# Kernel optimization log

Hardware: AMD Instinct MI355X
Metric: run time of the kernel (lower is better)

## Reference

```python
import jax, jax.numpy as jnp
import numpy as np

NUM_HEADS = 8
ROPE_MIN_LOG = -12.0
ROPE_MAX_LOG = 0.0
EPS = 1e-6


def rms_norm(h, w):
    # per-head-dim RMSNorm in fp32 (Qwen3 style), no shift applied in forward
    dt = h.dtype
    h32 = h.astype(jnp.float32)
    var = jnp.mean(h32 * h32, axis=-1, keepdims=True)
    return (w * (h32 * jax.lax.rsqrt(var + EPS))).astype(dt)


def setup_inputs() -> dict:
    key = jax.random.key(0)
    k1, k2, k3 = jax.random.split(key, 3)
    B, H, W, C = 1, 256, 256, 512
    x = jax.random.normal(k1, (B, H, W, C), dtype=jnp.float32)
    w_qkv = jax.random.normal(k2, (3 * C, C), dtype=jnp.float32) * 0.02
    hd = C // NUM_HEADS
    q_norm_w = jnp.ones((hd,), dtype=jnp.float32)
    k_norm_w = jnp.ones((hd,), dtype=jnp.float32)
    w_proj = jax.random.normal(k3, (C, C), dtype=jnp.float32) * 0.02
    b_proj = jnp.zeros((C,), dtype=jnp.float32)
    return {"x": x, "w_qkv": w_qkv, "q_norm_w": q_norm_w, "k_norm_w": k_norm_w,
            "w_proj": w_proj, "b_proj": b_proj}


def reference(x, w_qkv, q_norm_w, k_norm_w, w_proj, b_proj):
    B, H, W, C = x.shape
    nh = NUM_HEADS
    hd = C // nh
    rope_dim = (hd // 2) * 2
    half = rope_dim // 2
    scale = hd ** -0.5

    # [B,H,W,C] -> [B*W, H, C]
    xr = jnp.transpose(x, (0, 2, 1, 3)).reshape(B * W, H, C)
    qkv = jnp.einsum('bhc,dc->bhd', xr, w_qkv)                # [BW, H, 3C]
    qkv = qkv.reshape(B * W, H, 3, nh, hd)
    qkv = jnp.transpose(qkv, (2, 0, 3, 1, 4))                 # [3, BW, nh, H, hd]
    q, k, v = qkv[0], qkv[1], qkv[2]

    q = rms_norm(q, q_norm_w)
    k = rms_norm(k, k_norm_w)

    # segmented-exponential RoPE along trace axis H (default normalized pos)
    pos = jnp.linspace(0.0, 1.0, H, dtype=jnp.float32)        # [H]
    freqs = jnp.exp(jnp.linspace(ROPE_MIN_LOG, ROPE_MAX_LOG, half, dtype=jnp.float32))
    ang = pos[:, None] * freqs[None, :] * jnp.float32(H)      # [H, half]
    cos = jnp.cos(ang)
    sin = jnp.sin(ang)

    def rope(t):
        rot = t[..., :rope_dim].reshape(B * W, nh, H, half, 2)
        te, to = rot[..., 0], rot[..., 1]
        e2 = te * cos - to * sin
        o2 = te * sin + to * cos
        rot2 = jnp.stack([e2, o2], axis=-1).reshape(B * W, nh, H, rope_dim)
        return jnp.concatenate([rot2, t[..., rope_dim:]], axis=-1)

    q = rope(q)
    k = rope(k)

    # SDPA (non-causal, no dropout)
    scores = jnp.einsum('bnqd,bnkd->bnqk', q, k) * scale      # [BW, nh, H, H]
    attn = jax.nn.softmax(scores, axis=-1)
    o = jnp.einsum('bnqk,bnkd->bnqd', attn, v)                # [BW, nh, H, hd]

    o = jnp.transpose(o, (0, 2, 1, 3)).reshape(B * W, H, C)
    out = jnp.einsum('bhc,dc->bhd', o, w_proj) + b_proj
    out = out.reshape(B, W, H, C)
    return jnp.transpose(out, (0, 2, 1, 3))                   # [B, H, W, C]
```

## Files before the change

kernel.cpp:

```cpp
#include <hip/hip_runtime.h>
#include <hip/hip_bf16.h>
#include <cstdint>
#include <cstddef>

#define SEQ 256
#define WDIM 256
#define CDIM 512
#define NHEAD 8
#define HD 64
#define NTOK (SEQ*WDIM)
#define NTT 8

typedef __attribute__((ext_vector_type(8))) short bf16x8;
typedef __attribute__((ext_vector_type(4))) float f32x4;

static __device__ __forceinline__ unsigned short f2bf(float f) {
  __hip_bfloat16 h = __float2bfloat16(f);
  return *reinterpret_cast<unsigned short*>(&h);
}

__global__ void k_convert(const float* __restrict__ x,
                          const float* __restrict__ wqkv,
                          const float* __restrict__ wproj,
                          unsigned short* __restrict__ xb,
                          unsigned short* __restrict__ wqb,
                          unsigned short* __restrict__ wpb) {
  const int NX = NTOK*CDIM/4, NQ = 3*CDIM*CDIM/4, NP = CDIM*CDIM/4;
  const int total = NX + NQ + NP;
  for (int i = blockIdx.x*blockDim.x + threadIdx.x; i < total; i += gridDim.x*blockDim.x) {
    const float4* s; unsigned short* d; int j;
    if (i < NX)           { s = (const float4*)x;     d = xb;  j = i; }
    else if (i < NX+NQ)   { s = (const float4*)wqkv;  d = wqb; j = i-NX; }
    else                  { s = (const float4*)wproj; d = wpb; j = i-NX-NQ; }
    float4 f = s[j];
    ushort4 o;
    o.x = f2bf(f.x); o.y = f2bf(f.y); o.z = f2bf(f.z); o.w = f2bf(f.w);
    ((ushort4*)d)[j] = o;
  }
}

__global__ void k_rope(float2* __restrict__ tab) {
  int i = blockIdx.x*blockDim.x + threadIdx.x;
  if (i >= SEQ*32) return;
  int h = i >> 5, j = i & 31;
  float freq = expf(-12.0f + 12.0f*(float)j/31.0f);
  float ang = ((float)h/255.0f) * freq * 256.0f;
  tab[i] = make_float2(cosf(ang), sinf(ang));
}


#define STAGE_G(tau_, part_)                                                              \
  if ((tau_) < NTT) {                                                                     \
    const int buf_ = (tau_) & 1;                                                          \
    const int ab_ = (part_) >> 1, hh_ = (part_) & 1;                                      \
    const unsigned short* src_ = ab_ ? B : A;                                             \
    const int row0_ = (ab_ ? rowB0 : rowA0) + hh_*128;                                    \
    _Pragma("unroll")                                                                     \
    for (int c_ = 0; c_ < 2; ++c_) {                                                      \
      int G_ = wid*128 + c_*64 + lane;                                                    \
      int r_ = G_ >> 3, g_ = G_ & 7;                                                      \
      int gsw_ = g_ ^ (r_ & 7);                                                           \
      __builtin_amdgcn_global_load_lds(                                                   \
        (const __attribute__((address_space(1))) unsigned int*)                           \
          ((const char*)src_ + (size_t)(row0_ + r_)*1024 + (size_t)(tau_)*128 + gsw_*16), \
        (__attribute__((address_space(3))) unsigned int*)                                 \
          ((char*)&L[buf_][ab_][hh_][0] + G_*16),                                         \
        16, 0, 0);                                                                        \
    }                                                                                     \
  }

#define LDA_(dst, m_, kk_)                                                                 \
  { int r_ = (m_)*16 + li;                                                                 \
    dst = *(const bf16x8*)((const char*)&L[buf][0][wr][0] + r_*128 + (((((kk_)*4)+lg) ^ (r_ & 7))<<4)); }
#define LDB_(dst, n_, kk_)                                                                 \
  { int r_ = (wc & 1)*64 + (n_)*16 + li;                                                   \
    dst = *(const bf16x8*)((const char*)&L[buf][1][wc>>1][0] + r_*128 + (((((kk_)*4)+lg) ^ (r_ & 7))<<4)); }

#define PH_SYNC                                            \
  __builtin_amdgcn_s_barrier();                            \
  asm volatile("s_waitcnt lgkmcnt(0)" ::: "memory");       \
  __builtin_amdgcn_sched_barrier(0);

#define MFMA16(afr, bfr, mo)                                                               \
  __builtin_amdgcn_s_setprio(1);                                                          \
  _Pragma("unroll")                                                                        \
  for (int m = 0; m < 4; ++m)                                                              \
    _Pragma("unroll")                                                                      \
    for (int n = 0; n < 4; ++n)                                                            \
      acc[m+(mo)][n] = __builtin_amdgcn_mfma_f32_16x16x32_bf16(afr[m], bfr[n], acc[m+(mo)][n], 0, 0, 0); \
  __builtin_amdgcn_s_setprio(0);

__device__ __forceinline__ void gemm256(const unsigned short* __restrict__ A,
                                        const unsigned short* __restrict__ B,
                                        int rowA0, int rowB0,
                                        unsigned short (&L)[2][2][2][128*64],
                                        f32x4 (&acc)[8][4]) {
  const int tid = threadIdx.x;
  const int lane = tid & 63, wid = tid >> 6;
  const int wr = wid >> 2, wc = wid & 3;
  const int li = lane & 15, lg = lane >> 4;

  STAGE_G(0,0) STAGE_G(0,1) STAGE_G(0,2) STAGE_G(0,3) STAGE_G(1,0) STAGE_G(1,1)
  asm volatile("s_waitcnt vmcnt(4)" ::: "memory");
  __builtin_amdgcn_s_barrier();

  #pragma unroll 1
  for (int tau = 0; tau < NTT; ++tau) {
    const int buf = tau & 1;
    bf16x8 a0[4], a1[4], aL0[4], aL1[4], bb0[4], bb1[4];
    #pragma unroll
    for (int m = 0; m < 4; ++m) LDA_(a0[m], m, 0);
    #pragma unroll
    for (int n = 0; n < 4; ++n) LDB_(bb0[n], n, 0);
    STAGE_G(tau+1, 2)
    PH_SYNC
    MFMA16(a0, bb0, 0)
    __builtin_amdgcn_s_barrier();
    #pragma unroll
    for (int m = 0; m < 4; ++m) LDA_(a1[m], m+4, 0);
    #pragma unroll
    for (int m = 0; m < 4; ++m) LDA_(aL0[m], m, 1);
    STAGE_G(tau+1, 3)
    PH_SYNC
    MFMA16(a1, bb0, 4)
    __builtin_amdgcn_s_barrier();
    #pragma unroll
    for (int m = 0; m < 4; ++m) LDA_(aL1[m], m+4, 1);
    #pragma unroll
    for (int n = 0; n < 4; ++n) LDB_(bb1[n], n, 1);
    PH_SYNC
    MFMA16(aL0, bb1, 0)
    __builtin_amdgcn_s_barrier();
    STAGE_G(tau+2, 0)
    STAGE_G(tau+2, 1)
    __builtin_amdgcn_sched_barrier(0);
    MFMA16(aL1, bb1, 4)
    if (tau < NTT-2) { asm volatile("s_waitcnt vmcnt(4)" ::: "memory"); }
    else             { asm volatile("s_waitcnt vmcnt(0)" ::: "memory"); }
    __builtin_amdgcn_s_barrier();
  }
}

__launch_bounds__(512)
__global__ void k_qkv(const unsigned short* __restrict__ A,
                      const unsigned short* __restrict__ B,
                      const float* __restrict__ qnw, const float* __restrict__ knw,
                      const float2* __restrict__ rope,
                      unsigned short* __restrict__ Qw,
                      unsigned short* __restrict__ Kw,
                      unsigned short* __restrict__ Vw) {
  __shared__ __align__(16) unsigned short L[2][2][2][128*64];
  int wg = (blockIdx.x & 7)*192 + (blockIdx.x >> 3);
  int bn = wg % 6, bm = wg / 6;
  f32x4 acc[8][4] = {};
  gemm256(A, B, bm*256, bn*256, L, acc);

  const int lane = threadIdx.x & 63, wid = threadIdx.x >> 6;
  const int wr = wid >> 2, wc = wid & 3;
  const int li = lane & 15, lg = lane >> 4;
  int d0 = bn*256 + wc*64;
  int third = d0 >> 9;
  int nhh = (d0 >> 6) & 7;
  int t0 = bm*256 + wr*128;
  int hpos = bm;

  if (third == 2) {
    #pragma unroll
    for (int m = 0; m < 8; ++m)
      #pragma unroll
      for (int n = 0; n < 4; ++n)
        #pragma unroll
        for (int r = 0; r < 4; ++r) {
          int t = t0 + m*16 + lg*4 + r;
          int wI = t & 255;
          int e = n*16 + li;
          Vw[((size_t)(wI*8 + nhh)*256 + hpos)*64 + e] = f2bf(acc[m][n][r]);
        }
  } else {
    const float* nw = (third == 0) ? qnw : knw;
    unsigned short* dst = (third == 0) ? Qw : Kw;
    const float qsc = (third == 0) ? 0.125f : 1.0f;
    float nwv[4]; float2 cs[4];
    #pragma unroll
    for (int n = 0; n < 4; ++n) {
      int e = n*16 + li;
      nwv[n] = nw[e];
      cs[n] = rope[hpos*32 + (e >> 1)];
    }
    bool odd = (li & 1) != 0;
    #pragma unroll
    for (int m = 0; m < 8; ++m) {
      float rsg[4];
      #pragma unroll
      for (int r = 0; r < 4; ++r) {
        float p = 0.f;
        #pragma unroll
        for (int n = 0; n < 4; ++n) p += acc[m][n][r]*acc[m][n][r];
        #pragma unroll
        for (int d = 1; d < 16; d <<= 1) p += __shfl_xor(p, d, 64);
        rsg[r] = rsqrtf(p*(1.0f/64.0f) + 1e-6f);
      }
      #pragma unroll
      for (int n = 0; n < 4; ++n)
        #pragma unroll
        for (int r = 0; r < 4; ++r) {
          float v = acc[m][n][r] * rsg[r] * nwv[n];
          float pr = __shfl_xor(v, 1, 64);
          float res = odd ? (pr*cs[n].y + v*cs[n].x) : (v*cs[n].x - pr*cs[n].y);
          res *= qsc;
          int t = t0 + m*16 + lg*4 + r;
          int wI = t & 255;
          int e = n*16 + li;
          dst[((size_t)(wI*8 + nhh)*256 + hpos)*64 + e] = f2bf(res);
        }
    }
  }
}

__launch_bounds__(256, 2)
__global__ void k_attn(const unsigned short* __restrict__ Q,
                       const unsigned short* __restrict__ K,
                       const unsigned short* __restrict__ V,
                       unsigned short* __restrict__ O) {
  __shared__ __align__(16) unsigned short P_lds[4][64*64];
  __shared__ __align__(16) unsigned short VT_lds[64*72];
  int b = blockIdx.x;
  const unsigned short* Qb = Q + (size_t)b*SEQ*HD;
  const unsigned short* Kb = K + (size_t)b*SEQ*HD;
  const unsigned short* Vb = V + (size_t)b*SEQ*HD;
  const int lane = threadIdx.x & 63, wid = threadIdx.x >> 6;
  const int li = lane & 15, lg = lane >> 4;
  const int q0 = wid*64;
  char* Pw = (char*)&P_lds[wid][0];

  bf16x8 vrow[2];
  #pragma unroll
  for (int gi = 0; gi < 2; ++gi)
    vrow[gi] = *(const bf16x8*)(Vb + (size_t)lane*64 + (wid + gi*4)*8);

  bf16x8 qf[4][2];
  #pragma unroll
  for (int n = 0; n < 4; ++n)
    #pragma unroll
    for (int kk = 0; kk < 2; ++kk)
      qf[n][kk] = *(const bf16x8*)(Qb + (q0 + n*16 + li)*64 + kk*32 + lg*8);

  f32x4 oa[4][4] = {};
  float mrun[4], lrun[4];
  #pragma unroll
  for (int n = 0; n < 4; ++n) { mrun[n] = -1e30f; lrun[n] = 0.0f; }

  #pragma unroll 1
  for (int kb = 0; kb < 4; ++kb) {
    int key0 = kb*64;
    f32x4 s[4][4] = {};
    #pragma unroll
    for (int kk = 0; kk < 2; ++kk) {
      bf16x8 kf[4];
      #pragma unroll
      for (int m = 0; m < 4; ++m)
        kf[m] = *(const bf16x8*)(Kb + (key0 + m*16 + li)*64 + kk*32 + lg*8);
      __builtin_amdgcn_s_setprio(1);
      #pragma unroll
      for (int m = 0; m < 4; ++m)
        #pragma unroll
        for (int n = 0; n < 4; ++n)
          s[m][n] = __builtin_amdgcn_mfma_f32_16x16x32_bf16(kf[m], qf[n][kk], s[m][n], 0, 0, 0);
      __builtin_amdgcn_s_setprio(0);
    }
    float vmx[4];
    #pragma unroll
    for (int n = 0; n < 4; ++n) {
      float v = -1e30f;
      #pragma unroll
      for (int m = 0; m < 4; ++m)
        #pragma unroll
        for (int r = 0; r < 4; ++r) v = fmaxf(v, s[m][n][r]);
      v = fmaxf(v, __shfl_xor(v, 16, 64));
      v = fmaxf(v, __shfl_xor(v, 32, 64));
      vmx[n] = v;
    }
    float dmax = -1e30f;
    #pragma unroll
    for (int n = 0; n < 4; ++n) dmax = fmaxf(dmax, vmx[n] - mrun[n]);
    float mx[4];
    if (!__all(dmax <= 8.0f)) {
      float al[4];
      #pragma unroll
      for (int n = 0; n < 4; ++n) {
        float mn = fmaxf(mrun[n], vmx[n]);
        al[n] = __expf(mrun[n] - mn);
        mrun[n] = mn; mx[n] = mn;
        lrun[n] *= al[n];
      }
      #pragma unroll
      for (int mp = 0; mp < 4; ++mp)
        #pragma unroll
        for (int r = 0; r < 4; ++r) {
          float a = __shfl(al[mp], lg*4 + r, 64);
          #pragma unroll
          for (int np = 0; np < 4; ++np) oa[mp][np][r] *= a;
        }
    } else {
      #pragma unroll
      for (int n = 0; n < 4; ++n) mx[n] = mrun[n];
    }
    float rs[4] = {0.f,0.f,0.f,0.f};
    #pragma unroll
    for (int m = 0; m < 4; ++m)
      #pragma unroll
      for (int n = 0; n < 4; ++n) {
        f32x4 sv = s[m][n];
        #pragma unroll
        for (int r = 0; r < 4; ++r) {
          float p = __expf(sv[r] - mx[n]);
          sv[r] = p; rs[n] += p;
        }
        unsigned lo = (unsigned)f2bf(sv[0]) | ((unsigned)f2bf(sv[1]) << 16);
        unsigned hi = (unsigned)f2bf(sv[2]) | ((unsigned)f2bf(sv[3]) << 16);
        uint2 pk; pk.x = lo; pk.y = hi;
        int q = n*16 + li;
        int off = (q*128 + (m*16 + lg*4)*2) ^ ((li & 7) << 4);
        *(uint2*)(Pw + off) = pk;
      }
    #pragma unroll
    for (int n = 0; n < 4; ++n) {
      rs[n] += __shfl_xor(rs[n], 16, 64);
      rs[n] += __shfl_xor(rs[n], 32, 64);
      lrun[n] += rs[n];
    }
    __builtin_amdgcn_s_barrier();
    #pragma unroll
    for (int gi = 0; gi < 2; ++gi) {
      int g = wid + gi*4;
      #pragma unroll
      for (int j = 0; j < 8; ++j)
        VT_lds[(g*8 + j)*72 + lane] = (unsigned short)vrow[gi][j];
    }
    if (kb < 3) {
      #pragma unroll
      for (int gi = 0; gi < 2; ++gi)
        vrow[gi] = *(const bf16x8*)(Vb + (size_t)((kb+1)*64 + lane)*64 + (wid + gi*4)*8);
    }
    asm volatile("s_waitcnt lgkmcnt(0)" ::: "memory");
    __builtin_amdgcn_s_barrier();
    #pragma unroll
    for (int kk = 0; kk < 2; ++kk) {
      bf16x8 pf[4], vf[4];
      #pragma unroll
      for (int mp = 0; mp < 4; ++mp) {
        int q = mp*16 + li;
        int off = (q*128 + (kk*32 + lg*8)*2) ^ ((li & 7) << 4);
        pf[mp] = *(const bf16x8*)(Pw + off);
      }
      #pragma unroll
      for (int np = 0; np < 4; ++np)
        vf[np] = *(const bf16x8*)&VT_lds[(np*16 + li)*72 + kk*32 + lg*8];
      __builtin_amdgcn_s_setprio(1);
      #pragma unroll
      for (int mp = 0; mp < 4; ++mp)
        #pragma unroll
        for (int np = 0; np < 4; ++np)
          oa[mp][np] = __builtin_amdgcn_mfma_f32_16x16x32_bf16(pf[mp], vf[np], oa[mp][np], 0, 0, 0);
      __builtin_amdgcn_s_setprio(0);
    }
  }
  int wseq = b >> 3, whead = b & 7;
  #pragma unroll
  for (int mp = 0; mp < 4; ++mp)
    #pragma unroll
    for (int r = 0; r < 4; ++r) {
      float linv = 1.0f / __shfl(lrun[mp], lg*4 + r, 64);
      #pragma unroll
      for (int np = 0; np < 4; ++np) {
        int q = q0 + mp*16 + lg*4 + r;
        int e = np*16 + li;
        O[((size_t)q*WDIM + wseq)*CDIM + whead*HD + e] = f2bf(oa[mp][np][r] * linv);
      }
    }
}

__launch_bounds__(512)
__global__ void k_proj(const unsigned short* __restrict__ A,
                       const unsigned short* __restrict__ B,
                       const float* __restrict__ bias,
                       float* __restrict__ out) {
  __shared__ __align__(16) unsigned short L[2][2][2][128*64];
  int wg = (blockIdx.x & 7)*64 + (blockIdx.x >> 3);
  int bn = wg & 1, bm = wg >> 1;
  f32x4 acc[8][4] = {};
  gemm256(A, B, bm*256, bn*256, L, acc);

  const int lane = threadIdx.x & 63, wid = threadIdx.x >> 6;
  const int wr = wid >> 2, wc = wid & 3;
  const int li = lane & 15, lg = lane >> 4;
  int d0 = bn*256 + wc*64;
  int t0 = bm*256 + wr*128;
  float bi[4];
  #pragma unroll
  for (int n = 0; n < 4; ++n) bi[n] = bias[d0 + n*16 + li];
  #pragma unroll
  for (int m = 0; m < 8; ++m)
    #pragma unroll
    for (int n = 0; n < 4; ++n)
      #pragma unroll
      for (int r = 0; r < 4; ++r)
        out[(size_t)(t0 + m*16 + lg*4 + r)*CDIM + d0 + n*16 + li] = acc[m][n][r] + bi[n];
}

extern "C" void kernel_launch(void* const* d_in, const int* in_sizes, int n_in,
                              void* d_out, int out_size, void* d_ws, size_t ws_size,
                              hipStream_t stream) {
  (void)in_sizes; (void)n_in; (void)out_size; (void)ws_size;
  const float* x     = (const float*)d_in[0];
  const float* wqkv  = (const float*)d_in[1];
  const float* qnw   = (const float*)d_in[2];
  const float* knw   = (const float*)d_in[3];
  const float* wproj = (const float*)d_in[4];
  const float* bproj = (const float*)d_in[5];
  float* out = (float*)d_out;
  char* ws = (char*)d_ws;

  const size_t SZ_X = (size_t)NTOK*CDIM*2;
  unsigned short* xb  = (unsigned short*)(ws);
  unsigned short* wqb = (unsigned short*)(ws + SZ_X);
  unsigned short* wpb = (unsigned short*)(ws + SZ_X + 1572864);
  float2*         rp  = (float2*)       (ws + SZ_X + 1572864 + 524288);
  unsigned short* Qw  = (unsigned short*)(ws + SZ_X + 1572864 + 524288 + 65536);
  unsigned short* Kw  = (unsigned short*)((char*)Qw + SZ_X);
  unsigned short* Vw  = (unsigned short*)((char*)Kw + SZ_X);
  unsigned short* Ow  = xb;

  k_convert<<<dim3(2048), dim3(256), 0, stream>>>(x, wqkv, wproj, xb, wqb, wpb);
  k_rope   <<<dim3(32),   dim3(256), 0, stream>>>(rp);
  k_qkv    <<<dim3(1536), dim3(512), 0, stream>>>(xb, wqb, qnw, knw, rp, Qw, Kw, Vw);
  k_attn   <<<dim3(2048), dim3(256), 0, stream>>>(Qw, Kw, Vw, Ow);
  k_proj   <<<dim3(512),  dim3(512), 0, stream>>>(Ow, wpb, bproj, out);
}
```

Baseline: 322.8 us.

## Make QKV GEMM persistent over N tiles and double-buffer V transpose in attention

```diff
diff --git a/kernel.cpp b/kernel.cpp
--- a/kernel.cpp
+++ b/kernel.cpp
@@ -48,6 +48,27 @@
   tab[i] = make_float2(cosf(ang), sinf(ang));
 }
 
+
+#define LDA_(dst, m_, kk_)                                                                 \
+  { int r_ = (m_)*16 + li;                                                                 \
+    dst = *(const bf16x8*)((const char*)&L[buf][0][wr][0] + r_*128 + (((((kk_)*4)+lg) ^ (r_ & 7))<<4)); }
+#define LDB_(dst, n_, kk_)                                                                 \
+  { int r_ = (wc & 1)*64 + (n_)*16 + li;                                                   \
+    dst = *(const bf16x8*)((const char*)&L[buf][1][wc>>1][0] + r_*128 + (((((kk_)*4)+lg) ^ (r_ & 7))<<4)); }
+
+#define PH_SYNC                                            \
+  __builtin_amdgcn_s_barrier();                            \
+  asm volatile("s_waitcnt lgkmcnt(0)" ::: "memory");       \
+  __builtin_amdgcn_sched_barrier(0);
+
+#define MFMA16(afr, bfr, mo)                                                               \
+  __builtin_amdgcn_s_setprio(1);                                                          \
+  _Pragma("unroll")                                                                        \
+  for (int m = 0; m < 4; ++m)                                                              \
+    _Pragma("unroll")                                                                      \
+    for (int n = 0; n < 4; ++n)                                                            \
+      acc[m+(mo)][n] = __builtin_amdgcn_mfma_f32_16x16x32_bf16(afr[m], bfr[n], acc[m+(mo)][n], 0, 0, 0); \
+  __builtin_amdgcn_s_setprio(0);
 
 #define STAGE_G(tau_, part_)                                                              \
   if ((tau_) < NTT) {                                                                     \
@@ -69,27 +90,6 @@
     }                                                                                     \
   }
 
-#define LDA_(dst, m_, kk_)                                                                 \
-  { int r_ = (m_)*16 + li;                                                                 \
-    dst = *(const bf16x8*)((const char*)&L[buf][0][wr][0] + r_*128 + (((((kk_)*4)+lg) ^ (r_ & 7))<<4)); }
-#define LDB_(dst, n_, kk_)                                                                 \
-  { int r_ = (wc & 1)*64 + (n_)*16 + li;                                                   \
-    dst = *(const bf16x8*)((const char*)&L[buf][1][wc>>1][0] + r_*128 + (((((kk_)*4)+lg) ^ (r_ & 7))<<4)); }
-
-#define PH_SYNC                                            \
-  __builtin_amdgcn_s_barrier();                            \
-  asm volatile("s_waitcnt lgkmcnt(0)" ::: "memory");       \
-  __builtin_amdgcn_sched_barrier(0);
-
-#define MFMA16(afr, bfr, mo)                                                               \
-  __builtin_amdgcn_s_setprio(1);                                                          \
-  _Pragma("unroll")                                                                        \
-  for (int m = 0; m < 4; ++m)                                                              \
-    _Pragma("unroll")                                                                      \
-    for (int n = 0; n < 4; ++n)                                                            \
-      acc[m+(mo)][n] = __builtin_amdgcn_mfma_f32_16x16x32_bf16(afr[m], bfr[n], acc[m+(mo)][n], 0, 0, 0); \
-  __builtin_amdgcn_s_setprio(0);
-
 __device__ __forceinline__ void gemm256(const unsigned short* __restrict__ A,
                                         const unsigned short* __restrict__ B,
                                         int rowA0, int rowB0,
@@ -141,6 +141,89 @@
   }
 }
 
+
+#define STAGE_P(tau_, part_)                                                              \
+  if ((tau_) < NTP) {                                                                     \
+    const int buf_ = (tau_) & 1, Tk_ = (tau_) & 7;                                        \
+    const int ab_ = (part_) >> 1, hh_ = (part_) & 1;                                      \
+    const unsigned short* src_ = ab_ ? B : A;                                             \
+    const int row0_ = (ab_ ? ((tau_) >> 3)*256 : rowA0) + hh_*128;                        \
+    _Pragma("unroll")                                                                     \
+    for (int c_ = 0; c_ < 2; ++c_) {                                                      \
+      int G_ = wid*128 + c_*64 + lane;                                                    \
+      int r_ = G_ >> 3, g_ = G_ & 7;                                                      \
+      int gsw_ = g_ ^ (r_ & 7);                                                           \
+      __builtin_amdgcn_global_load_lds(                                                   \
+        (const __attribute__((address_space(1))) unsigned int*)                           \
+          ((const char*)src_ + (size_t)(row0_ + r_)*1024 + (size_t)Tk_*128 + gsw_*16),    \
+        (__attribute__((address_space(3))) unsigned int*)                                 \
+          ((char*)&L[buf_][ab_][hh_][0] + G_*16),                                         \
+        16, 0, 0);                                                                        \
+    }                                                                                     \
+  }
+
+template<int NB, class EPI>
+__device__ __forceinline__ void gemm_persist(const unsigned short* __restrict__ A,
+                                             const unsigned short* __restrict__ B,
+                                             int rowA0,
+                                             unsigned short (&L)[2][2][2][128*64],
+                                             EPI&& epi) {
+  constexpr int NTP = NB * 8;
+  const int tid = threadIdx.x;
+  const int lane = tid & 63, wid = tid >> 6;
+  const int wr = wid >> 2, wc = wid & 3;
+  const int li = lane & 15, lg = lane >> 4;
+
+  STAGE_P(0,0) STAGE_P(0,1) STAGE_P(0,2) STAGE_P(0,3) STAGE_P(1,0) STAGE_P(1,1)
+  asm volatile("s_waitcnt vmcnt(4)" ::: "memory");
+  __builtin_amdgcn_s_barrier();
+
+  f32x4 acc[8][4] = {};
+  #pragma unroll 1
+  for (int tau = 0; tau < NTP; ++tau) {
+    const int buf = tau & 1;
+    bf16x8 a0[4], a1[4], aL0[4], aL1[4], bb0[4], bb1[4];
+    #pragma unroll
+    for (int m = 0; m < 4; ++m) LDA_(a0[m], m, 0);
+    #pragma unroll
+    for (int n = 0; n < 4; ++n) LDB_(bb0[n], n, 0);
+    STAGE_P(tau+1, 2)
+    PH_SYNC
+    MFMA16(a0, bb0, 0)
+    __builtin_amdgcn_s_barrier();
+    #pragma unroll
+    for (int m = 0; m < 4; ++m) LDA_(a1[m], m+4, 0);
+    #pragma unroll
+    for (int m = 0; m < 4; ++m) LDA_(aL0[m], m, 1);
+    STAGE_P(tau+1, 3)
+    PH_SYNC
+    MFMA16(a1, bb0, 4)
+    __builtin_amdgcn_s_barrier();
+    #pragma unroll
+    for (int m = 0; m < 4; ++m) LDA_(aL1[m], m+4, 1);
+    #pragma unroll
+    for (int n = 0; n < 4; ++n) LDB_(bb1[n], n, 1);
+    PH_SYNC
+    MFMA16(aL0, bb1, 0)
+    __builtin_amdgcn_s_barrier();
+    STAGE_P(tau+2, 0)
+    STAGE_P(tau+2, 1)
+    __builtin_amdgcn_sched_barrier(0);
+    MFMA16(aL1, bb1, 4)
+    if (tau < NTP-2) { asm volatile("s_waitcnt vmcnt(4)" ::: "memory"); }
+    else             { asm volatile("s_waitcnt vmcnt(0)" ::: "memory"); }
+    __builtin_amdgcn_s_barrier();
+    if ((tau & 7) == 7) {
+      epi(tau >> 3, acc);
+      #pragma unroll
+      for (int m = 0; m < 8; ++m)
+        #pragma unroll
+        for (int n = 0; n < 4; ++n)
+          acc[m][n] = (f32x4){0.f,0.f,0.f,0.f};
+    }
+  }
+}
+
 __launch_bounds__(512)
 __global__ void k_qkv(const unsigned short* __restrict__ A,
                       const unsigned short* __restrict__ B,
@@ -150,71 +233,69 @@
                       unsigned short* __restrict__ Kw,
                       unsigned short* __restrict__ Vw) {
   __shared__ __align__(16) unsigned short L[2][2][2][128*64];
-  int wg = (blockIdx.x & 7)*192 + (blockIdx.x >> 3);
-  int bn = wg % 6, bm = wg / 6;
-  f32x4 acc[8][4] = {};
-  gemm256(A, B, bm*256, bn*256, L, acc);
-
+  const int bm = blockIdx.x;
   const int lane = threadIdx.x & 63, wid = threadIdx.x >> 6;
   const int wr = wid >> 2, wc = wid & 3;
   const int li = lane & 15, lg = lane >> 4;
-  int d0 = bn*256 + wc*64;
-  int third = d0 >> 9;
-  int nhh = (d0 >> 6) & 7;
-  int t0 = bm*256 + wr*128;
-  int hpos = bm;
-
-  if (third == 2) {
-    #pragma unroll
-    for (int m = 0; m < 8; ++m)
-      #pragma unroll
-      for (int n = 0; n < 4; ++n)
+  const int t0 = bm*256 + wr*128;
+  const int hpos = bm;
+  float2 cs[4]; float qn[4], kn[4];
+  #pragma unroll
+  for (int n = 0; n < 4; ++n) {
+    int e = n*16 + li;
+    cs[n] = rope[hpos*32 + (e >> 1)];
+    qn[n] = qnw[e]; kn[n] = knw[e];
+  }
+  const bool odd = (li & 1) != 0;
+
+  gemm_persist<6>(A, B, bm*256, L, [&](int j, f32x4 (&acc)[8][4]) {
+    int d0 = j*256 + wc*64;
+    int third = d0 >> 9;
+    int nhh = (d0 >> 6) & 7;
+    if (third == 2) {
+      #pragma unroll
+      for (int m = 0; m < 8; ++m)
+        #pragma unroll
+        for (int n = 0; n < 4; ++n)
+          #pragma unroll
+          for (int r = 0; r < 4; ++r) {
+            int t = t0 + m*16 + lg*4 + r;
+            int wI = t & 255;
+            int e = n*16 + li;
+            Vw[((size_t)(wI*8 + nhh)*256 + hpos)*64 + e] = f2bf(acc[m][n][r]);
+          }
+    } else {
+      const float* nw = (third == 0) ? qn : kn;
+      unsigned short* dst = (third == 0) ? Qw : Kw;
+      const float qsc = (third == 0) ? 0.125f : 1.0f;
+      #pragma unroll
+      for (int m = 0; m < 8; ++m) {
+        float rsg[4];
         #pragma unroll
         for (int r = 0; r < 4; ++r) {
-          int t = t0 + m*16 + lg*4 + r;
-          int wI = t & 255;
-          int e = n*16 + li;
-          Vw[((size_t)(wI*8 + nhh)*256 + hpos)*64 + e] = f2bf(acc[m][n][r]);
+          float p = 0.f;
+          #pragma unroll
+          for (int n = 0; n < 4; ++n) p += acc[m][n][r]*acc[m][n][r];
+          #pragma unroll
+          for (int d = 1; d < 16; d <<= 1) p += __shfl_xor(p, d, 64);
+          rsg[r] = rsqrtf(p*(1.0f/64.0f) + 1e-6f);
         }
-  } else {
-    const float* nw = (third == 0) ? qnw : knw;
-    unsigned short* dst = (third == 0) ? Qw : Kw;
-    const float qsc = (third == 0) ? 0.125f : 1.0f;
-    float nwv[4]; float2 cs[4];
-    #pragma unroll
-    for (int n = 0; n < 4; ++n) {
-      int e = n*16 + li;
-      nwv[n] = nw[e];
-      cs[n] = rope[hpos*32 + (e >> 1)];
-    }
-    bool odd = (li & 1) != 0;
-    #pragma unroll
-    for (int m = 0; m < 8; ++m) {
-      float rsg[4];
-      #pragma unroll
-      for (int r = 0; r < 4; ++r) {
-        float p = 0.f;
-        #pragma unroll
-        for (int n = 0; n < 4; ++n) p += acc[m][n][r]*acc[m][n][r];
-        #pragma unroll
-        for (int d = 1; d < 16; d <<= 1) p += __shfl_xor(p, d, 64);
-        rsg[r] = rsqrtf(p*(1.0f/64.0f) + 1e-6f);
-      }
-      #pragma unroll
-      for (int n = 0; n < 4; ++n)
-        #pragma unroll
-        for (int r = 0; r < 4; ++r) {
-          float v = acc[m][n][r] * rsg[r] * nwv[n];
-          float pr = __shfl_xor(v, 1, 64);
-          float res = odd ? (pr*cs[n].y + v*cs[n].x) : (v*cs[n].x - pr*cs[n].y);
-          res *= qsc;
-          int t = t0 + m*16 + lg*4 + r;
-          int wI = t & 255;
-          int e = n*16 + li;
-          dst[((size_t)(wI*8 + nhh)*256 + hpos)*64 + e] = f2bf(res);
-        }
-    }
-  }
+        #pragma unroll
+        for (int n = 0; n < 4; ++n)
+          #pragma unroll
+          for (int r = 0; r < 4; ++r) {
+            float v = acc[m][n][r] * rsg[r] * nw[n];
+            float pr = __shfl_xor(v, 1, 64);
+            float res = odd ? (pr*cs[n].y + v*cs[n].x) : (v*cs[n].x - pr*cs[n].y);
+            res *= qsc;
+            int t = t0 + m*16 + lg*4 + r;
+            int wI = t & 255;
+            int e = n*16 + li;
+            dst[((size_t)(wI*8 + nhh)*256 + hpos)*64 + e] = f2bf(res);
+          }
+      }
+    }
+  });
 }
 
 __launch_bounds__(256, 2)
@@ -223,7 +304,7 @@
                        const unsigned short* __restrict__ V,
                        unsigned short* __restrict__ O) {
   __shared__ __align__(16) unsigned short P_lds[4][64*64];
-  __shared__ __align__(16) unsigned short VT_lds[64*72];
+  __shared__ __align__(16) unsigned short VT_lds[2][64*72];
   int b = blockIdx.x;
   const unsigned short* Qb = Q + (size_t)b*SEQ*HD;
   const unsigned short* Kb = K + (size_t)b*SEQ*HD;
@@ -237,6 +318,16 @@
   #pragma unroll
   for (int gi = 0; gi < 2; ++gi)
     vrow[gi] = *(const bf16x8*)(Vb + (size_t)lane*64 + (wid + gi*4)*8);
+  #pragma unroll
+  for (int gi = 0; gi < 2; ++gi) {
+    int g = wid + gi*4;
+    #pragma unroll
+    for (int j = 0; j < 8; ++j)
+      VT_lds[0][(g*8 + j)*72 + lane] = (unsigned short)vrow[gi][j];
+  }
+  #pragma unroll
+  for (int gi = 0; gi < 2; ++gi)
+    vrow[gi] = *(const bf16x8*)(Vb + (size_t)(64 + lane)*64 + (wid + gi*4)*8);
 
   bf16x8 qf[4][2];
   #pragma unroll
@@ -329,21 +420,22 @@
       rs[n] += __shfl_xor(rs[n], 32, 64);
       lrun[n] += rs[n];
     }
-    __builtin_amdgcn_s_barrier();
-    #pragma unroll
-    for (int gi = 0; gi < 2; ++gi) {
-      int g = wid + gi*4;
-      #pragma unroll
-      for (int j = 0; j < 8; ++j)
-        VT_lds[(g*8 + j)*72 + lane] = (unsigned short)vrow[gi][j];
-    }
+    asm volatile("s_waitcnt lgkmcnt(0)" ::: "memory");
+    __builtin_amdgcn_s_barrier();
     if (kb < 3) {
       #pragma unroll
-      for (int gi = 0; gi < 2; ++gi)
-        vrow[gi] = *(const bf16x8*)(Vb + (size_t)((kb+1)*64 + lane)*64 + (wid + gi*4)*8);
-    }
-    asm volatile("s_waitcnt lgkmcnt(0)" ::: "memory");
-    __builtin_amdgcn_s_barrier();
+      for (int gi = 0; gi < 2; ++gi) {
+        int g = wid + gi*4;
+        #pragma unroll
+        for (int j = 0; j < 8; ++j)
+          VT_lds[(kb+1)&1][(g*8 + j)*72 + lane] = (unsigned short)vrow[gi][j];
+      }
+      if (kb < 2) {
+        #pragma unroll
+        for (int gi = 0; gi < 2; ++gi)
+          vrow[gi] = *(const bf16x8*)(Vb + (size_t)((kb+2)*64 + lane)*64 + (wid + gi*4)*8);
+      }
+    }
     #pragma unroll
     for (int kk = 0; kk < 2; ++kk) {
       bf16x8 pf[4], vf[4];
@@ -355,7 +447,7 @@
       }
       #pragma unroll
       for (int np = 0; np < 4; ++np)
-        vf[np] = *(const bf16x8*)&VT_lds[(np*16 + li)*72 + kk*32 + lg*8];
+        vf[np] = *(const bf16x8*)&VT_lds[kb&1][(np*16 + li)*72 + kk*32 + lg*8];
       __builtin_amdgcn_s_setprio(1);
       #pragma unroll
       for (int mp = 0; mp < 4; ++mp)
@@ -433,7 +525,7 @@
 
   k_convert<<<dim3(2048), dim3(256), 0, stream>>>(x, wqkv, wproj, xb, wqb, wpb);
   k_rope   <<<dim3(32),   dim3(256), 0, stream>>>(rp);
-  k_qkv    <<<dim3(1536), dim3(512), 0, stream>>>(xb, wqb, qnw, knw, rp, Qw, Kw, Vw);
+  k_qkv    <<<dim3(256),  dim3(512), 0, stream>>>(xb, wqb, qnw, knw, rp, Qw, Kw, Vw);
   k_attn   <<<dim3(2048), dim3(256), 0, stream>>>(Qw, Kw, Vw, Ow);
   k_proj   <<<dim3(512),  dim3(512), 0, stream>>>(Ow, wpb, bproj, out);
 }
```

After: 316.0 us. 1.02x faster.
